# Performance work log

Measured on AMD Instinct MI355X. Metric: run time of the kernel, lower is better.

Reference implementation:

```python
import jax, jax.numpy as jnp
import numpy as np

DIM = 1024
HEADS = 16
HEAD_DIM = DIM // HEADS
HIDDEN = 4 * DIM
EPS = 1e-6


def _layer_norm(x, scale, bias):
    mu = jnp.mean(x, axis=-1, keepdims=True)
    var = jnp.mean(jnp.square(x - mu), axis=-1, keepdims=True)
    return (x - mu) * jax.lax.rsqrt(var + EPS) * scale + bias


def setup_inputs() -> dict:
    key = jax.random.key(0)
    ks = jax.random.split(key, 8)
    s = 0.02
    return {
        "x": jax.random.normal(ks[0], (8, 1024, DIM), dtype=jnp.float32),
        "w_qkv": jax.random.normal(ks[1], (DIM, 3 * DIM), dtype=jnp.float32) * s,
        "b_qkv": jnp.zeros((3 * DIM,), jnp.float32),
        "w_proj": jax.random.normal(ks[2], (DIM, DIM), dtype=jnp.float32) * s,
        "b_proj": jnp.zeros((DIM,), jnp.float32),
        "ln1_scale": jnp.ones((DIM,), jnp.float32),
        "ln1_bias": jnp.zeros((DIM,), jnp.float32),
        "ln2_scale": jnp.ones((DIM,), jnp.float32),
        "ln2_bias": jnp.zeros((DIM,), jnp.float32),
        "w_fc1": jax.random.normal(ks[3], (DIM, HIDDEN), dtype=jnp.float32) * s,
        "b_fc1": jnp.zeros((HIDDEN,), jnp.float32),
        "w_fc2": jax.random.normal(ks[4], (HIDDEN, DIM), dtype=jnp.float32) * s,
        "b_fc2": jnp.zeros((DIM,), jnp.float32),
    }


def reference(x, w_qkv, b_qkv, w_proj, b_proj, ln1_scale, ln1_bias,
              ln2_scale, ln2_bias, w_fc1, b_fc1, w_fc2, b_fc2):
    B, N, C = x.shape
    scale = HEAD_DIM ** -0.5

    # --- attention branch ---
    h = _layer_norm(x, ln1_scale, ln1_bias)
    qkv = h @ w_qkv + b_qkv                          # [B,N,3C]
    qkv = qkv.reshape(B, N, 3, HEADS, HEAD_DIM)
    qkv = jnp.transpose(qkv, (2, 0, 3, 1, 4))        # [3,B,H,N,D]
    q, k, v = qkv[0], qkv[1], qkv[2]
    attn = jnp.einsum("bhnd,bhmd->bhnm", q, k) * scale
    attn = jax.nn.softmax(attn, axis=-1)
    o = jnp.einsum("bhnm,bhmd->bhnd", attn, v)       # [B,H,N,D]
    o = jnp.transpose(o, (0, 2, 1, 3)).reshape(B, N, C)
    x = x + (o @ w_proj + b_proj)

    # --- mlp branch ---
    h = _layer_norm(x, ln2_scale, ln2_bias)
    h = jax.nn.gelu(h @ w_fc1 + b_fc1)               # tanh approx, matches flax default
    x = x + (h @ w_fc2 + b_fc2)
    return x
```

## Files before the change

kernel.cpp:

```cpp
#include <hip/hip_runtime.h>

typedef __attribute__((ext_vector_type(8))) short short8;
typedef __attribute__((ext_vector_type(4))) float f32x4;
typedef unsigned short ushort;
typedef unsigned int uint;

#define DIM 1024
#define NSEQ 1024
#define BATCH 8
#define HEADS 16
#define HD 64
#define HIDDEN 4096
#define NROWS (BATCH * NSEQ)

__device__ inline ushort f2bf(float f) {
  uint u = __float_as_uint(f);
  u += 0x7fff + ((u >> 16) & 1);
  return (ushort)(u >> 16);
}

__device__ inline f32x4 zero4() {
  f32x4 z; z[0] = 0.f; z[1] = 0.f; z[2] = 0.f; z[3] = 0.f; return z;
}

__device__ inline float gelu_fast(float x) {
  float u2 = 1.5957691216057308f * (x + 0.044715f * x * x * x);
  float e = __builtin_amdgcn_exp2f(-1.4426950408889634f * u2);
  return x / (1.0f + e);
}

#define GLDS16(g, l)                                                  \
  __builtin_amdgcn_global_load_lds(                                   \
      (const __attribute__((address_space(1))) void*)(g),             \
      (__attribute__((address_space(3))) void*)(l), 16, 0, 0)

#define WAITVM(n) asm volatile("s_waitcnt vmcnt(" #n ")" ::: "memory")
#define SBAR() asm volatile("s_barrier" ::: "memory")

__global__ __launch_bounds__(256) void ln_kernel(
    const float* __restrict__ x, const float* __restrict__ sc,
    const float* __restrict__ bi, ushort* __restrict__ out) {
  int row = blockIdx.x;
  int t = threadIdx.x;
  const float4 v = reinterpret_cast<const float4*>(x + (size_t)row * DIM)[t];
  float s = v.x + v.y + v.z + v.w;
  float s2 = v.x * v.x + v.y * v.y + v.z * v.z + v.w * v.w;
#pragma unroll
  for (int off = 32; off >= 1; off >>= 1) {
    s += __shfl_xor(s, off);
    s2 += __shfl_xor(s2, off);
  }
  __shared__ float ps[4], ps2[4];
  int w = t >> 6;
  if ((t & 63) == 0) { ps[w] = s; ps2[w] = s2; }
  __syncthreads();
  s = ps[0] + ps[1] + ps[2] + ps[3];
  s2 = ps2[0] + ps2[1] + ps2[2] + ps2[3];
  float mu = s * (1.0f / DIM);
  float var = s2 * (1.0f / DIM) - mu * mu;
  float rstd = rsqrtf(var + 1e-6f);
  float4 scv = reinterpret_cast<const float4*>(sc)[t];
  float4 biv = reinterpret_cast<const float4*>(bi)[t];
  ushort4 o;
  o.x = f2bf((v.x - mu) * rstd * scv.x + biv.x);
  o.y = f2bf((v.y - mu) * rstd * scv.y + biv.y);
  o.z = f2bf((v.z - mu) * rstd * scv.z + biv.z);
  o.w = f2bf((v.w - mu) * rstd * scv.w + biv.w);
  reinterpret_cast<ushort4*>(out + (size_t)row * DIM)[t] = o;
}

__global__ __launch_bounds__(256) void wtrans_kernel(
    const float* __restrict__ w, ushort* __restrict__ wt, int K, int N) {
  __shared__ float tile[32][33];
  int n0 = blockIdx.x * 32, k0 = blockIdx.y * 32;
  int tx = threadIdx.x & 31, ty = threadIdx.x >> 5;
#pragma unroll
  for (int j = 0; j < 4; j++)
    tile[ty + 8 * j][tx] = w[(size_t)(k0 + ty + 8 * j) * N + n0 + tx];
  __syncthreads();
#pragma unroll
  for (int j = 0; j < 4; j++)
    wt[(size_t)(n0 + ty + 8 * j) * K + k0 + tx] = f2bf(tile[tx][ty + 8 * j]);
}

__global__ __launch_bounds__(256) void vtrans_kernel(
    const ushort* __restrict__ qkv, ushort* __restrict__ vT) {
  __shared__ ushort Ts[64 * 64];
  int bh = blockIdx.y;
  int b = bh >> 4, h = bh & 15;
  int n0 = blockIdx.x * 64;
  int t = threadIdx.x;
  const ushort* src = qkv + (size_t)b * NSEQ * 3072 + 2048 + h * 64;
#pragma unroll
  for (int i = 0; i < 2; i++) {
    int ci = i * 256 + t;
    int rr = ci >> 3, c = ci & 7;
    short8 v = *reinterpret_cast<const short8*>(src + (size_t)(n0 + rr) * 3072 + c * 8);
    *reinterpret_cast<short8*>(&Ts[rr * 64 + ((c ^ (rr >> 3)) & 7) * 8]) = v;
  }
  __syncthreads();
  ushort* dst = vT + (size_t)bh * 64 * NSEQ;
#pragma unroll
  for (int i = 0; i < 2; i++) {
    int ci = i * 256 + t;
    int dd = ci >> 3, c = ci & 7;
    short8 v;
#pragma unroll
    for (int j = 0; j < 8; j++) {
      int nn = c * 8 + j;
      v[j] = (short)Ts[nn * 64 + (((dd >> 3) ^ (nn >> 3)) & 7) * 8 + (dd & 7)];
    }
    *reinterpret_cast<short8*>(dst + (size_t)dd * NSEQ + n0 + c * 8) = v;
  }
}

template <int BN, int EPI, int KK>
__global__ __launch_bounds__(512, 2) void gemm256_kernel(
    const ushort* __restrict__ A, const ushort* __restrict__ Bt,
    const float* __restrict__ bias, const float* __restrict__ res,
    void* __restrict__ outp, int M, int N) {
  constexpr int BM = 256, BK = 32;
  constexpr int WM = (BN == 256) ? 2 : 4;
  constexpr int WN = 8 / WM;
  constexpr int MR = (BM / WM) / 16;
  constexpr int NR = (BN / WN) / 16;
  constexpr int AR = 2;
  constexpr int BR = BN / 128;
  constexpr int nkt = KK / BK;
  static_assert(BN == 256 || BN == 128, "");
  static_assert(nkt >= 4 && (nkt % 2) == 0, "");

  __shared__ ushort As[4][BM * BK];
  __shared__ ushort Bs[4][BN * BK];

  int t = threadIdx.x, lane = t & 63, w = t >> 6;
  int wr = w / WN, wc = w % WN;
  int r = lane & 15, g = lane >> 4;

  int nwg = gridDim.x * gridDim.y;
  int flat = blockIdx.y * gridDim.x + blockIdx.x;
  int swzf = (flat & 7) * (nwg >> 3) + (flat >> 3);
  int bx = swzf % gridDim.x, by = swzf / gridDim.x;
  int m0 = by * BM, n0 = bx * BN;

  const ushort* Ab = A + (size_t)m0 * KK;
  const ushort* Bb = Bt + (size_t)n0 * KK;

  int srow = t >> 2;
  int sgc8 = (((t & 3) ^ (srow & 3) ^ ((srow >> 2) & 3)) & 3) * 8;
  int swb = (w << 4) * BK;
  int sw = ((g ^ (r & 3) ^ ((r >> 2) & 3)) & 3) * 8;

  auto stageAB = [&](int kt2) {
    ushort* as = &As[kt2 & 3][0];
    ushort* bs = &Bs[kt2 & 3][0];
    int ko = kt2 * BK;
#pragma unroll
    for (int p = 0; p < AR; p++)
      GLDS16(Ab + (size_t)(p * 128 + srow) * KK + ko + sgc8,
             as + p * 128 * BK + swb);
#pragma unroll
    for (int p = 0; p < BR; p++)
      GLDS16(Bb + (size_t)(p * 128 + srow) * KK + ko + sgc8,
             bs + p * 128 * BK + swb);
  };

  auto ldfrags = [&](int kt2, short8 (&fa_)[MR], short8 (&fb_)[NR]) {
    const ushort* as = &As[kt2 & 3][0];
    const ushort* bs = &Bs[kt2 & 3][0];
#pragma unroll
    for (int mi = 0; mi < MR; mi++)
      fa_[mi] = *reinterpret_cast<const short8*>(
          &as[(wr * (BM / WM) + mi * 16 + r) * BK + sw]);
#pragma unroll
    for (int ni = 0; ni < NR; ni++)
      fb_[ni] = *reinterpret_cast<const short8*>(
          &bs[(wc * (BN / WN) + ni * 16 + r) * BK + sw]);
  };

  f32x4 acc[MR][NR];
#pragma unroll
  for (int mi = 0; mi < MR; mi++)
#pragma unroll
    for (int ni = 0; ni < NR; ni++) acc[mi][ni] = zero4();

  auto body = [&](int kt, short8 (&ca)[MR], short8 (&cb)[NR],
                  short8 (&na)[MR], short8 (&nb)[NR]) {
    if (kt + 1 < nkt) ldfrags(kt + 1, na, nb);
    if (kt + 3 < nkt) stageAB(kt + 3);
    __builtin_amdgcn_s_setprio(1);
#pragma unroll
    for (int mi = 0; mi < MR; mi++)
#pragma unroll
      for (int ni = 0; ni < NR; ni++)
        acc[mi][ni] = __builtin_amdgcn_mfma_f32_16x16x32_bf16(
            ca[mi], cb[ni], acc[mi][ni], 0, 0, 0);
    __builtin_amdgcn_s_setprio(0);
    if (kt + 3 < nkt) {
      if constexpr (BN == 256) WAITVM(4); else WAITVM(3);
      SBAR();
    } else if (kt + 2 < nkt) {
      WAITVM(0);
      SBAR();
    }
  };

  stageAB(0); stageAB(1); stageAB(2);
  if constexpr (BN == 256) WAITVM(4); else WAITVM(3);
  SBAR();

  short8 fa[2][MR], fb[2][NR];
  ldfrags(0, fa[0], fb[0]);
#pragma unroll 1
  for (int k2 = 0; k2 < nkt / 2; k2++) {
    body(2 * k2 + 0, fa[0], fb[0], fa[1], fb[1]);
    body(2 * k2 + 1, fa[1], fb[1], fa[0], fb[0]);
  }

  int rg = g * 4;
#pragma unroll
  for (int mi = 0; mi < MR; mi++) {
#pragma unroll
    for (int ni = 0; ni < NR; ni++) {
      int row = m0 + wr * (BM / WM) + mi * 16 + rg;
      int col = n0 + wc * (BN / WN) + ni * 16 + r;
      float bv = bias[col];
#pragma unroll
      for (int j = 0; j < 4; j++) {
        float v = acc[mi][ni][j] + bv;
        if (EPI == 1) v = gelu_fast(v);
        if (EPI == 2) {
          reinterpret_cast<float*>(outp)[(size_t)(row + j) * N + col] =
              v + res[(size_t)(row + j) * N + col];
        } else {
          reinterpret_cast<ushort*>(outp)[(size_t)(row + j) * N + col] = f2bf(v);
        }
      }
    }
  }
}

template <int EPI>
__global__ __launch_bounds__(256, 3) void gemm128_kernel(
    const ushort* __restrict__ A, const ushort* __restrict__ Bt,
    const float* __restrict__ bias, const float* __restrict__ res,
    void* __restrict__ outp, int M, int N, int K) {
  constexpr int BM = 128, BN = 128, BK = 32;

  __shared__ ushort As[2][BM * BK];
  __shared__ ushort Bs[2][BN * BK];

  int t = threadIdx.x, lane = t & 63, w = t >> 6;
  int wr = w >> 1, wc = w & 1;
  int r = lane & 15, g = lane >> 4;

  int nwg = gridDim.x * gridDim.y;
  int flat = blockIdx.y * gridDim.x + blockIdx.x;
  int swzf = (flat & 7) * (nwg >> 3) + (flat >> 3);
  int bx = swzf % gridDim.x, by = swzf / gridDim.x;
  int m0 = by * BM, n0 = bx * BN;

  const ushort* Ab = A + (size_t)m0 * K;
  const ushort* Bb = Bt + (size_t)n0 * K;

  int srow = t >> 2;
  int sgc8 = (((t & 3) ^ (srow & 3) ^ ((srow >> 2) & 3)) & 3) * 8;
  int swb = (t >> 6) * 16 * BK;
  int sw = ((g ^ (r & 3) ^ ((r >> 2) & 3)) & 3) * 8;

  f32x4 acc[4][4];
#pragma unroll
  for (int mi = 0; mi < 4; mi++)
#pragma unroll
    for (int ni = 0; ni < 4; ni++) acc[mi][ni] = zero4();

  int nkt = K / BK;
#pragma unroll
  for (int p = 0; p < 2; p++) {
    GLDS16(Ab + (size_t)(p * 64 + srow) * K + sgc8, &As[0][(p * 64) * BK + swb]);
    GLDS16(Bb + (size_t)(p * 64 + srow) * K + sgc8, &Bs[0][(p * 64) * BK + swb]);
  }
  __syncthreads();

  int cur = 0;
  for (int kt = 0; kt < nkt; kt++) {
    if (kt + 1 < nkt) {
      int ko = (kt + 1) * BK;
#pragma unroll
      for (int p = 0; p < 2; p++) {
        GLDS16(Ab + (size_t)(p * 64 + srow) * K + ko + sgc8,
               &As[cur ^ 1][(p * 64) * BK + swb]);
        GLDS16(Bb + (size_t)(p * 64 + srow) * K + ko + sgc8,
               &Bs[cur ^ 1][(p * 64) * BK + swb]);
      }
    }
    short8 a[4], b[4];
#pragma unroll
    for (int mi = 0; mi < 4; mi++)
      a[mi] = *reinterpret_cast<const short8*>(
          &As[cur][(wr * 64 + mi * 16 + r) * BK + sw]);
#pragma unroll
    for (int ni = 0; ni < 4; ni++)
      b[ni] = *reinterpret_cast<const short8*>(
          &Bs[cur][(wc * 64 + ni * 16 + r) * BK + sw]);
#pragma unroll
    for (int mi = 0; mi < 4; mi++)
#pragma unroll
      for (int ni = 0; ni < 4; ni++)
        acc[mi][ni] = __builtin_amdgcn_mfma_f32_16x16x32_bf16(
            a[mi], b[ni], acc[mi][ni], 0, 0, 0);
    __syncthreads();
    cur ^= 1;
  }

  int rg = g * 4;
#pragma unroll
  for (int mi = 0; mi < 4; mi++) {
#pragma unroll
    for (int ni = 0; ni < 4; ni++) {
      int row = m0 + wr * 64 + mi * 16 + rg;
      int col = n0 + wc * 64 + ni * 16 + r;
      float bv = bias[col];
#pragma unroll
      for (int j = 0; j < 4; j++) {
        float v = acc[mi][ni][j] + bv;
        if (EPI == 1) v = gelu_fast(v);
        if (EPI == 2) {
          reinterpret_cast<float*>(outp)[(size_t)(row + j) * N + col] =
              v + res[(size_t)(row + j) * N + col];
        } else {
          reinterpret_cast<ushort*>(outp)[(size_t)(row + j) * N + col] = f2bf(v);
        }
      }
    }
  }
}

#define SM_SCALE_L2E 0.18033688f
#define SM_BIAS_L2E 11.54156036f
__global__ __launch_bounds__(256) void attn_kernel(
    const ushort* __restrict__ qkv, const ushort* __restrict__ vT,
    ushort* __restrict__ o) {
  __shared__ ushort Kt[64 * 72];
  __shared__ ushort Vt[64 * 72];
  __shared__ ushort Pl[4][16 * 72];
  int q0 = blockIdx.x * 64, h = blockIdx.y, b = blockIdx.z;
  int t = threadIdx.x, lane = t & 63, w = t >> 6;
  int r = lane & 15, g = lane >> 4;
  const ushort* base = qkv + (size_t)b * NSEQ * 3072 + h * 64;
  const ushort* vbase = vT + (size_t)(b * HEADS + h) * 64 * NSEQ;

  short8 qf[2];
  {
    const ushort* qrow = base + (size_t)(q0 + w * 16 + r) * 3072;
    qf[0] = *reinterpret_cast<const short8*>(qrow + g * 8);
    qf[1] = *reinterpret_cast<const short8*>(qrow + 32 + g * 8);
  }

  float l[4] = {0.f, 0.f, 0.f, 0.f};
  f32x4 oacc[4];
#pragma unroll
  for (int db = 0; db < 4; db++) oacc[db] = zero4();

  int srw = t >> 3, sc8 = (t & 7) * 8;
  for (int kt = 0; kt < NSEQ / 64; kt++) {
    int k0 = kt * 64;
    short8 kreg[2], vreg[2];
#pragma unroll
    for (int i = 0; i < 2; i++) {
      int rw = srw + i * 32;
      kreg[i] = *reinterpret_cast<const short8*>(base + 1024 + (size_t)(k0 + rw) * 3072 + sc8);
      vreg[i] = *reinterpret_cast<const short8*>(vbase + (size_t)rw * NSEQ + k0 + sc8);
    }
    __syncthreads();
#pragma unroll
    for (int i = 0; i < 2; i++) {
      int rw = srw + i * 32;
      *reinterpret_cast<short8*>(&Kt[rw * 72 + sc8]) = kreg[i];
      *reinterpret_cast<short8*>(&Vt[rw * 72 + sc8]) = vreg[i];
    }
    __syncthreads();

#pragma unroll
    for (int kb = 0; kb < 4; kb++) {
      short8 kf0 = *reinterpret_cast<const short8*>(&Kt[(kb * 16 + r) * 72 + g * 8]);
      short8 kf1 = *reinterpret_cast<const short8*>(&Kt[(kb * 16 + r) * 72 + 32 + g * 8]);
      f32x4 z = zero4();
      z = __builtin_amdgcn_mfma_f32_16x16x32_bf16(qf[0], kf0, z, 0, 0, 0);
      z = __builtin_amdgcn_mfma_f32_16x16x32_bf16(qf[1], kf1, z, 0, 0, 0);
#pragma unroll
      for (int j = 0; j < 4; j++) {
        float p = __builtin_amdgcn_exp2f(fmaf(z[j], SM_SCALE_L2E, -SM_BIAS_L2E));
        l[j] += p;
        Pl[w][(g * 4 + j) * 72 + kb * 16 + r] = (ushort)(__float_as_uint(p) >> 16);
      }
    }

#pragma unroll
    for (int ks = 0; ks < 2; ks++) {
      short8 pa = *reinterpret_cast<const short8*>(&Pl[w][r * 72 + ks * 32 + g * 8]);
#pragma unroll
      for (int db = 0; db < 4; db++) {
        short8 vb = *reinterpret_cast<const short8*>(&Vt[(db * 16 + r) * 72 + ks * 32 + g * 8]);
        oacc[db] = __builtin_amdgcn_mfma_f32_16x16x32_bf16(pa, vb, oacc[db], 0, 0, 0);
      }
    }
  }

#pragma unroll
  for (int j = 0; j < 4; j++) {
#pragma unroll
    for (int off = 8; off >= 1; off >>= 1) l[j] += __shfl_xor(l[j], off);
    l[j] = 1.0f / l[j];
  }

#pragma unroll
  for (int db = 0; db < 4; db++)
#pragma unroll
    for (int j = 0; j < 4; j++) {
      size_t row = (size_t)b * NSEQ + q0 + w * 16 + g * 4 + j;
      int col = h * 64 + db * 16 + r;
      o[row * DIM + col] = f2bf(oacc[db][j] * l[j]);
    }
}

extern "C" void kernel_launch(void* const* d_in, const int* in_sizes, int n_in,
                              void* d_out, int out_size, void* d_ws, size_t ws_size,
                              hipStream_t stream) {
  const float* x      = (const float*)d_in[0];
  const float* w_qkv  = (const float*)d_in[1];
  const float* b_qkv  = (const float*)d_in[2];
  const float* w_proj = (const float*)d_in[3];
  const float* b_proj = (const float*)d_in[4];
  const float* ln1s   = (const float*)d_in[5];
  const float* ln1b   = (const float*)d_in[6];
  const float* ln2s   = (const float*)d_in[7];
  const float* ln2b   = (const float*)d_in[8];
  const float* w_fc1  = (const float*)d_in[9];
  const float* b_fc1  = (const float*)d_in[10];
  const float* w_fc2  = (const float*)d_in[11];
  const float* b_fc2  = (const float*)d_in[12];
  float* out = (float*)d_out;

  char* ws = (char*)d_ws;
  ushort* wqkv_t  = (ushort*)(ws);
  ushort* wproj_t = (ushort*)(ws + 6291456);
  ushort* wfc1_t  = (ushort*)(ws + 8388608);
  ushort* wfc2_t  = (ushort*)(ws + 16777216);
  ushort* hbuf    = (ushort*)(ws + 25165824);
  float*  x1      = (float*)(ws + 41943040);
  ushort* vTb     = (ushort*)(ws + 41943040);
  ushort* qkv     = (ushort*)(ws + 75497472);
  ushort* obuf    = (ushort*)(ws + 125829120);
  ushort* fc1a    = qkv;

  wtrans_kernel<<<dim3(3072 / 32, 1024 / 32), 256, 0, stream>>>(w_qkv, wqkv_t, 1024, 3072);
  wtrans_kernel<<<dim3(1024 / 32, 1024 / 32), 256, 0, stream>>>(w_proj, wproj_t, 1024, 1024);
  wtrans_kernel<<<dim3(4096 / 32, 1024 / 32), 256, 0, stream>>>(w_fc1, wfc1_t, 1024, 4096);
  wtrans_kernel<<<dim3(1024 / 32, 4096 / 32), 256, 0, stream>>>(w_fc2, wfc2_t, 4096, 1024);

  ln_kernel<<<NROWS, 256, 0, stream>>>(x, ln1s, ln1b, hbuf);
  gemm256_kernel<128, 0, 1024><<<dim3(3072 / 128, NROWS / 256), 512, 0, stream>>>(
      hbuf, wqkv_t, b_qkv, nullptr, qkv, NROWS, 3072);
  vtrans_kernel<<<dim3(NSEQ / 64, BATCH * HEADS), 256, 0, stream>>>(qkv, vTb);
  attn_kernel<<<dim3(NSEQ / 64, HEADS, BATCH), 256, 0, stream>>>(qkv, vTb, obuf);
  gemm256_kernel<128, 2, 1024><<<dim3(1024 / 128, NROWS / 256), 512, 0, stream>>>(
      obuf, wproj_t, b_proj, x, x1, NROWS, 1024);

  ln_kernel<<<NROWS, 256, 0, stream>>>(x1, ln2s, ln2b, hbuf);
  gemm128_kernel<1><<<dim3(4096 / 128, NROWS / 128), 256, 0, stream>>>(
      hbuf, wfc1_t, b_fc1, nullptr, fc1a, NROWS, 4096, 1024);
  gemm256_kernel<128, 2, 4096><<<dim3(1024 / 128, NROWS / 256), 512, 0, stream>>>(
      fc1a, wfc2_t, b_fc2, x1, out, NROWS, 1024);
}
```

Before: 397.8 us.

## Triple-buffer gemm128 loads and merge four weight-transpose launches into one

The fc1 GEMM kernel moves from double to triple-buffered LDS staging. It prefetches two K-tiles ahead and uses explicit vmcnt waits with raw barriers in place of __syncthreads, so global-to-LDS loads overlap more MFMA work. Separately, the four weight transpose/bf16-convert launches are fused into one launch that picks the weight by block index, saving three launch overheads. The extra LDS buffer raises shared memory per block, which may reduce occupancy under launch_bounds(256,3).

```diff
diff --git a/kernel.cpp b/kernel.cpp
--- a/kernel.cpp
+++ b/kernel.cpp
@@ -69,10 +69,27 @@
   reinterpret_cast<ushort4*>(out + (size_t)row * DIM)[t] = o;
 }
 
-__global__ __launch_bounds__(256) void wtrans_kernel(
-    const float* __restrict__ w, ushort* __restrict__ wt, int K, int N) {
+__global__ __launch_bounds__(256) void wtrans4_kernel(
+    const float* __restrict__ w_qkv, ushort* __restrict__ wqkv_t,
+    const float* __restrict__ w_proj, ushort* __restrict__ wproj_t,
+    const float* __restrict__ w_fc1, ushort* __restrict__ wfc1_t,
+    const float* __restrict__ w_fc2, ushort* __restrict__ wfc2_t) {
+  int b = blockIdx.x;
+  const float* w; ushort* wt; int K, N, bx, by;
+  if (b < 3072) {
+    w = w_qkv; wt = wqkv_t; K = 1024; N = 3072; bx = b % 96; by = b / 96;
+  } else if (b < 4096) {
+    int i = b - 3072;
+    w = w_proj; wt = wproj_t; K = 1024; N = 1024; bx = i % 32; by = i / 32;
+  } else if (b < 8192) {
+    int i = b - 4096;
+    w = w_fc1; wt = wfc1_t; K = 1024; N = 4096; bx = i % 128; by = i / 128;
+  } else {
+    int i = b - 8192;
+    w = w_fc2; wt = wfc2_t; K = 4096; N = 1024; bx = i % 32; by = i / 32;
+  }
   __shared__ float tile[32][33];
-  int n0 = blockIdx.x * 32, k0 = blockIdx.y * 32;
+  int n0 = bx * 32, k0 = by * 32;
   int tx = threadIdx.x & 31, ty = threadIdx.x >> 5;
 #pragma unroll
   for (int j = 0; j < 4; j++)
@@ -247,8 +264,8 @@
     void* __restrict__ outp, int M, int N, int K) {
   constexpr int BM = 128, BN = 128, BK = 32;
 
-  __shared__ ushort As[2][BM * BK];
-  __shared__ ushort Bs[2][BN * BK];
+  __shared__ ushort As[3][BM * BK];
+  __shared__ ushort Bs[3][BN * BK];
 
   int t = threadIdx.x, lane = t & 63, w = t >> 6;
   int wr = w >> 1, wc = w & 1;
@@ -268,6 +285,19 @@
   int swb = (t >> 6) * 16 * BK;
   int sw = ((g ^ (r & 3) ^ ((r >> 2) & 3)) & 3) * 8;
 
+  auto stage = [&](int kt2) {
+    ushort* as = &As[kt2 % 3][0];
+    ushort* bs = &Bs[kt2 % 3][0];
+    int ko = kt2 * BK;
+#pragma unroll
+    for (int p = 0; p < 2; p++) {
+      GLDS16(Ab + (size_t)(p * 64 + srow) * K + ko + sgc8,
+             as + (p * 64) * BK + swb);
+      GLDS16(Bb + (size_t)(p * 64 + srow) * K + ko + sgc8,
+             bs + (p * 64) * BK + swb);
+    }
+  };
+
   f32x4 acc[4][4];
 #pragma unroll
   for (int mi = 0; mi < 4; mi++)
@@ -275,42 +305,36 @@
     for (int ni = 0; ni < 4; ni++) acc[mi][ni] = zero4();
 
   int nkt = K / BK;
-#pragma unroll
-  for (int p = 0; p < 2; p++) {
-    GLDS16(Ab + (size_t)(p * 64 + srow) * K + sgc8, &As[0][(p * 64) * BK + swb]);
-    GLDS16(Bb + (size_t)(p * 64 + srow) * K + sgc8, &Bs[0][(p * 64) * BK + swb]);
-  }
-  __syncthreads();
-
-  int cur = 0;
+  stage(0); stage(1);
+  WAITVM(4);
+  SBAR();
+
   for (int kt = 0; kt < nkt; kt++) {
-    if (kt + 1 < nkt) {
-      int ko = (kt + 1) * BK;
-#pragma unroll
-      for (int p = 0; p < 2; p++) {
-        GLDS16(Ab + (size_t)(p * 64 + srow) * K + ko + sgc8,
-               &As[cur ^ 1][(p * 64) * BK + swb]);
-        GLDS16(Bb + (size_t)(p * 64 + srow) * K + ko + sgc8,
-               &Bs[cur ^ 1][(p * 64) * BK + swb]);
-      }
-    }
+    if (kt + 2 < nkt) stage(kt + 2);
+    const ushort* as = &As[kt % 3][0];
+    const ushort* bs = &Bs[kt % 3][0];
     short8 a[4], b[4];
 #pragma unroll
     for (int mi = 0; mi < 4; mi++)
       a[mi] = *reinterpret_cast<const short8*>(
-          &As[cur][(wr * 64 + mi * 16 + r) * BK + sw]);
+          &as[(wr * 64 + mi * 16 + r) * BK + sw]);
 #pragma unroll
     for (int ni = 0; ni < 4; ni++)
       b[ni] = *reinterpret_cast<const short8*>(
-          &Bs[cur][(wc * 64 + ni * 16 + r) * BK + sw]);
+          &bs[(wc * 64 + ni * 16 + r) * BK + sw]);
 #pragma unroll
     for (int mi = 0; mi < 4; mi++)
 #pragma unroll
       for (int ni = 0; ni < 4; ni++)
         acc[mi][ni] = __builtin_amdgcn_mfma_f32_16x16x32_bf16(
             a[mi], b[ni], acc[mi][ni], 0, 0, 0);
-    __syncthreads();
-    cur ^= 1;
+    if (kt + 2 < nkt) {
+      WAITVM(4);
+      SBAR();
+    } else if (kt + 1 < nkt) {
+      WAITVM(0);
+      SBAR();
+    }
   }
 
   int rg = g * 4;
@@ -454,10 +478,8 @@
   ushort* obuf    = (ushort*)(ws + 125829120);
   ushort* fc1a    = qkv;
 
-  wtrans_kernel<<<dim3(3072 / 32, 1024 / 32), 256, 0, stream>>>(w_qkv, wqkv_t, 1024, 3072);
-  wtrans_kernel<<<dim3(1024 / 32, 1024 / 32), 256, 0, stream>>>(w_proj, wproj_t, 1024, 1024);
-  wtrans_kernel<<<dim3(4096 / 32, 1024 / 32), 256, 0, stream>>>(w_fc1, wfc1_t, 1024, 4096);
-  wtrans_kernel<<<dim3(1024 / 32, 4096 / 32), 256, 0, stream>>>(w_fc2, wfc2_t, 4096, 1024);
+  wtrans4_kernel<<<12288, 256, 0, stream>>>(
+      w_qkv, wqkv_t, w_proj, wproj_t, w_fc1, wfc1_t, w_fc2, wfc2_t);
 
   ln_kernel<<<NROWS, 256, 0, stream>>>(x, ln1s, ln1b, hbuf);
   gemm256_kernel<128, 0, 1024><<<dim3(3072 / 128, NROWS / 256), 512, 0, stream>>>(
```

New measurement: 400.2 us. Within noise of the previous version (+0.6%).
